# Kernel tuning notes

Hardware: AMD Instinct MI355X
Metric: run time of the kernel (lower is better)

The kernel has to match this reference:

```python
import jax, jax.numpy as jnp
import numpy as np
import math

D_MODEL = 640
HEAD_DIM = 64
N_HEADS = 14
N_KV_HEADS = 2
HPK = N_HEADS // N_KV_HEADS  # 7
EPS = 1e-5
T = 2048
D_HALF = HEAD_DIM // 2


def setup_inputs() -> dict:
    key = jax.random.key(0)
    ks = jax.random.split(key, 10)
    x = jax.random.normal(ks[0], (1, D_MODEL, 1, T), dtype=jnp.float32)
    # rope tables: realistic cos/sin from standard rotary frequencies
    inv_freq = 1.0 / (10000.0 ** (jnp.arange(0, HEAD_DIM, 2, dtype=jnp.float32) / HEAD_DIM))
    ang = jnp.arange(T, dtype=jnp.float32)[:, None] * inv_freq[None, :]  # (T, 32)
    rope_cos = jnp.cos(ang)
    rope_sin = jnp.sin(ang)
    # causal additive mask (T, T)
    causal = jnp.tril(jnp.ones((T, T), dtype=bool))
    attn_mask = jnp.where(causal, 0.0, -1e9).astype(jnp.float32)
    norm_w = 1.0 + 0.02 * jax.random.normal(ks[1], (D_MODEL,), dtype=jnp.float32)
    qkv_dim = (N_HEADS + 2 * N_KV_HEADS) * HEAD_DIM  # 1152
    qkv_w = jax.random.normal(ks[2], (qkv_dim, D_MODEL), dtype=jnp.float32) * (D_MODEL ** -0.5)
    qkv_b = 0.02 * jax.random.normal(ks[3], (qkv_dim,), dtype=jnp.float32)
    o_w = jax.random.normal(ks[4], (D_MODEL, N_HEADS * HEAD_DIM), dtype=jnp.float32) * ((N_HEADS * HEAD_DIM) ** -0.5)
    o_b = 0.02 * jax.random.normal(ks[5], (D_MODEL,), dtype=jnp.float32)
    sinks = jax.random.normal(ks[6], (N_HEADS,), dtype=jnp.float32)
    return {"x": x, "rope_cos": rope_cos, "rope_sin": rope_sin, "attn_mask": attn_mask,
            "norm_w": norm_w, "qkv_w": qkv_w, "qkv_b": qkv_b, "o_w": o_w, "o_b": o_b,
            "sinks": sinks}


def _apply_rope(xf, n_heads, rope_cos, rope_sin):
    # xf: (1, T, n_heads*dh) -> interleaved rotary
    xr = xf.reshape(1, T, n_heads, HEAD_DIM)
    x1 = xr[..., 0::2]  # (1, T, n, d_half)
    x2 = xr[..., 1::2]
    cos = rope_cos[None, :, None, :]
    sin = rope_sin[None, :, None, :]
    o1 = x1 * cos - x2 * sin
    o2 = x2 * cos + x1 * sin
    return jnp.stack((o1, o2), axis=-1).reshape(1, T, n_heads * HEAD_DIM)


def reference(x, rope_cos, rope_sin, attn_mask, norm_w, qkv_w, qkv_b, o_w, o_b, sinks):
    nh, nkv, hpk, dh = N_HEADS, N_KV_HEADS, HPK, HEAD_DIM
    residual = x
    # RMSNorm over channel dim (axis=1)
    var = jnp.mean(x * x, axis=1, keepdims=True)
    normed = x * jax.lax.rsqrt(var + EPS) * norm_w.reshape(1, -1, 1, 1)
    # fused 1x1 conv QKV: (1, D, T) -> (1, T, qkv_dim)
    n2 = normed[:, :, 0, :]  # (1, D, T)
    qkv = jnp.einsum('bct,oc->bto', n2, qkv_w) + qkv_b
    q_dim = nh * dh
    kv_dim = nkv * dh
    q = qkv[:, :, :q_dim]
    k = qkv[:, :, q_dim:q_dim + kv_dim]
    v = qkv[:, :, q_dim + kv_dim:]
    q = _apply_rope(q, nh, rope_cos, rope_sin)
    k = _apply_rope(k, nkv, rope_cos, rope_sin)
    qk_scale = 1.0 / math.sqrt(math.sqrt(dh))
    q = q * qk_scale
    k = k * qk_scale
    q = q.reshape(1, T, nkv, hpk, dh)
    k = k.reshape(1, T, nkv, dh)
    v = v.reshape(1, T, nkv, dh)
    # GQA scores: (1, nkv, hpk, T, T)
    scores = jnp.einsum('btkgd,bskd->bkgts', q, k)
    scores = scores + attn_mask[None, None, None, :, :]
    # attention-sink logit column appended before softmax
    sink = (sinks * math.log(2.0)).reshape(1, nkv, hpk, 1, 1)
    sink_col = jnp.broadcast_to(sink, (1, nkv, hpk, T, 1))
    scores_with_sink = jnp.concatenate([scores, sink_col], axis=-1)
    attn_w = jax.nn.softmax(scores_with_sink, axis=-1)[..., :-1]
    # weighted values: (1, T, nkv, hpk, dh) -> (1, T, nh*dh)
    attn_out = jnp.einsum('bkgts,bskd->btkgd', attn_w, v).reshape(1, T, nh * dh)
    # output 1x1 conv + residual
    proj = jnp.einsum('bto,do->bdt', attn_out, o_w) + o_b.reshape(1, -1, 1)
    return residual + proj[:, :, None, :]
```

## Files before the change

kernel.cpp:

```cpp
#include <hip/hip_runtime.h>
#include <math.h>

#define T 2048
#define DM 640
#define NH 14
#define NKV 2
#define HPK 7
#define HD 64
#define QDIM 896
#define QKV_DIM 1152

constexpr float QK_SCALE = 0.35355339059327373f;
constexpr float LN2F = 0.6931471805599453f;
constexpr float EPSF = 1e-5f;

typedef __attribute__((ext_vector_type(8))) short short8;
typedef __attribute__((ext_vector_type(4))) float float4v;

static __device__ __forceinline__ unsigned short f2bf(float f) {
    union { float f; unsigned u; } v; v.f = f;
    unsigned r = v.u + 0x7fffu + ((v.u >> 16) & 1u);
    return (unsigned short)(r >> 16);
}
static __device__ __forceinline__ float bf2f(unsigned short s) {
    union { unsigned u; float f; } v; v.u = ((unsigned)s) << 16;
    return v.f;
}

__global__ __launch_bounds__(256) void rstd_partial_kernel(
    const float* __restrict__ x, float* __restrict__ rpart)
{
    const int t = blockIdx.x * 256 + threadIdx.x;
    const int cb = blockIdx.y;
    float ss = 0.f;
    #pragma unroll 8
    for (int i = 0; i < 64; ++i) {
        float v = x[(cb * 64 + i) * T + t];
        ss = fmaf(v, v, ss);
    }
    rpart[cb * T + t] = ss;
}

__global__ __launch_bounds__(256) void rstd_final_kernel(
    const float* __restrict__ rpart, float* __restrict__ rstd)
{
    const int t = blockIdx.x * 256 + threadIdx.x;
    float ss = 0.f;
    #pragma unroll
    for (int j = 0; j < 10; ++j) ss += rpart[j * T + t];
    rstd[t] = rsqrtf(ss * (1.0f / DM) + EPSF);
}

__global__ __launch_bounds__(256) void cast_hilo_kernel(
    const float* __restrict__ in, unsigned short* __restrict__ hi,
    unsigned short* __restrict__ lo, int n4)
{
    for (int i = blockIdx.x * 256 + threadIdx.x; i < n4; i += gridDim.x * 256) {
        const float4 v = ((const float4*)in)[i];
        ushort4 h, l;
        h.x = f2bf(v.x); l.x = f2bf(v.x - bf2f(h.x));
        h.y = f2bf(v.y); l.y = f2bf(v.y - bf2f(h.y));
        h.z = f2bf(v.z); l.z = f2bf(v.z - bf2f(h.z));
        h.w = f2bf(v.w); l.w = f2bf(v.w - bf2f(h.w));
        ((ushort4*)hi)[i] = h;
        ((ushort4*)lo)[i] = l;
    }
}

__global__ __launch_bounds__(256) void xnorm_kernel(
    const float* __restrict__ x, const float* __restrict__ norm_w,
    const float* __restrict__ rstd,
    unsigned short* __restrict__ XnH, unsigned short* __restrict__ XnL)
{
    const int tid = threadIdx.x;
    const int t0 = blockIdx.x * 64;
    const int c0 = blockIdx.y * 64;
    __shared__ float xs[64][65];

    #pragma unroll
    for (int it = 0; it < 4; ++it) {
        const int r = (tid >> 4) + it * 16;
        const int cl = (tid & 15) * 4;
        const float4 v = *(const float4*)&x[(size_t)(c0 + r) * T + t0 + cl];
        xs[r][cl + 0] = v.x; xs[r][cl + 1] = v.y;
        xs[r][cl + 2] = v.z; xs[r][cl + 3] = v.w;
    }
    __syncthreads();
    #pragma unroll
    for (int it = 0; it < 4; ++it) {
        const int tr = (tid >> 4) + it * 16;
        const int cl = (tid & 15) * 4;
        const float rs = rstd[t0 + tr];
        ushort4 h, l;
        float v0 = xs[cl + 0][tr] * norm_w[c0 + cl + 0] * rs;
        float v1 = xs[cl + 1][tr] * norm_w[c0 + cl + 1] * rs;
        float v2 = xs[cl + 2][tr] * norm_w[c0 + cl + 2] * rs;
        float v3 = xs[cl + 3][tr] * norm_w[c0 + cl + 3] * rs;
        h.x = f2bf(v0); l.x = f2bf(v0 - bf2f(h.x));
        h.y = f2bf(v1); l.y = f2bf(v1 - bf2f(h.y));
        h.z = f2bf(v2); l.z = f2bf(v2 - bf2f(h.z));
        h.w = f2bf(v3); l.w = f2bf(v3 - bf2f(h.w));
        *(ushort4*)&XnH[(size_t)(t0 + tr) * DM + c0 + cl] = h;
        *(ushort4*)&XnL[(size_t)(t0 + tr) * DM + c0 + cl] = l;
    }
}

#define QSX_H 0
#define QSX_L 8192
#define QSW_H 16384
#define QSW_L 24576

__global__ __launch_bounds__(256) void qkv_mfma_kernel(
    const unsigned short* __restrict__ XnH, const unsigned short* __restrict__ XnL,
    const unsigned short* __restrict__ WH, const unsigned short* __restrict__ WL,
    const float* __restrict__ qkv_b, const float* __restrict__ rope_cos,
    const float* __restrict__ rope_sin,
    unsigned short* __restrict__ Qh, unsigned short* __restrict__ Ql,
    unsigned short* __restrict__ Kh, unsigned short* __restrict__ Kl,
    unsigned short* __restrict__ Vth, unsigned short* __restrict__ Vtl)
{
    const int t0 = blockIdx.x * 64;
    const int o0 = blockIdx.y * 64;
    const int tid = threadIdx.x;
    const int wave = tid >> 6, lane = tid & 63;
    const int lg = lane >> 4, lq = lane & 15;
    const int wr = wave >> 1, wc = wave & 1;

    __shared__ __align__(16) unsigned char sm[32768];

    float4v acc[2][2];
    acc[0][0] = (float4v)0.f; acc[0][1] = (float4v)0.f;
    acc[1][0] = (float4v)0.f; acc[1][1] = (float4v)0.f;

    for (int c0 = 0; c0 < DM; c0 += 64) {
        __syncthreads();
        #pragma unroll
        for (int rep = 0; rep < 2; ++rep) {
            const int ci = tid + rep * 256;
            const int row = ci >> 3, cc = ci & 7;
            const int dst = row * 128 + ((cc * 16) ^ ((row & 7) << 4));
            *(uint4*)(sm + QSX_H + dst) = *(const uint4*)&XnH[(size_t)(t0 + row) * DM + c0 + cc * 8];
            *(uint4*)(sm + QSX_L + dst) = *(const uint4*)&XnL[(size_t)(t0 + row) * DM + c0 + cc * 8];
            *(uint4*)(sm + QSW_H + dst) = *(const uint4*)&WH[(size_t)(o0 + row) * DM + c0 + cc * 8];
            *(uint4*)(sm + QSW_L + dst) = *(const uint4*)&WL[(size_t)(o0 + row) * DM + c0 + cc * 8];
        }
        __syncthreads();
        #pragma unroll
        for (int kk = 0; kk < 2; ++kk) {
            short8 ah[2], al[2], bh[2], bl[2];
            #pragma unroll
            for (int nt = 0; nt < 2; ++nt) {
                const int row = wc * 32 + nt * 16 + lq;
                const int col = (kk * 64 + lg * 16) ^ ((row & 7) << 4);
                bh[nt] = *(const short8*)(sm + QSX_H + row * 128 + col);
                bl[nt] = *(const short8*)(sm + QSX_L + row * 128 + col);
            }
            #pragma unroll
            for (int mt = 0; mt < 2; ++mt) {
                const int row = wr * 32 + mt * 16 + lq;
                const int col = (kk * 64 + lg * 16) ^ ((row & 7) << 4);
                ah[mt] = *(const short8*)(sm + QSW_H + row * 128 + col);
                al[mt] = *(const short8*)(sm + QSW_L + row * 128 + col);
            }
            #pragma unroll
            for (int mt = 0; mt < 2; ++mt) {
                #pragma unroll
                for (int nt = 0; nt < 2; ++nt) {
                    acc[mt][nt] = __builtin_amdgcn_mfma_f32_16x16x32_bf16(ah[mt], bh[nt], acc[mt][nt], 0, 0, 0);
                    acc[mt][nt] = __builtin_amdgcn_mfma_f32_16x16x32_bf16(ah[mt], bl[nt], acc[mt][nt], 0, 0, 0);
                    acc[mt][nt] = __builtin_amdgcn_mfma_f32_16x16x32_bf16(al[mt], bh[nt], acc[mt][nt], 0, 0, 0);
                }
            }
        }
    }

    const int by = blockIdx.y;
    #pragma unroll
    for (int mt = 0; mt < 2; ++mt) {
        const int d0 = wr * 32 + mt * 16 + lg * 4;
        #pragma unroll
        for (int nt = 0; nt < 2; ++nt) {
            const int t = t0 + wc * 32 + nt * 16 + lq;
            if (by < 16) {
                const float e0 = acc[mt][nt][0] + qkv_b[o0 + d0 + 0];
                const float d1 = acc[mt][nt][1] + qkv_b[o0 + d0 + 1];
                const float e2 = acc[mt][nt][2] + qkv_b[o0 + d0 + 2];
                const float d3 = acc[mt][nt][3] + qkv_b[o0 + d0 + 3];
                const float c0v = rope_cos[t * 32 + (d0 >> 1)];
                const float s0v = rope_sin[t * 32 + (d0 >> 1)];
                const float c1v = rope_cos[t * 32 + (d0 >> 1) + 1];
                const float s1v = rope_sin[t * 32 + (d0 >> 1) + 1];
                const float r0 = (e0 * c0v - d1 * s0v) * QK_SCALE;
                const float r1 = (d1 * c0v + e0 * s0v) * QK_SCALE;
                const float r2 = (e2 * c1v - d3 * s1v) * QK_SCALE;
                const float r3 = (d3 * c1v + e2 * s1v) * QK_SCALE;
                ushort4 h, l;
                h.x = f2bf(r0); l.x = f2bf(r0 - bf2f(h.x));
                h.y = f2bf(r1); l.y = f2bf(r1 - bf2f(h.y));
                h.z = f2bf(r2); l.z = f2bf(r2 - bf2f(h.z));
                h.w = f2bf(r3); l.w = f2bf(r3 - bf2f(h.w));
                if (by < 14) {
                    *(ushort4*)&Qh[((size_t)(by * T + t)) * HD + d0] = h;
                    *(ushort4*)&Ql[((size_t)(by * T + t)) * HD + d0] = l;
                } else {
                    const int h2 = by - 14;
                    *(ushort4*)&Kh[((size_t)(h2 * T + t)) * HD + d0] = h;
                    *(ushort4*)&Kl[((size_t)(h2 * T + t)) * HD + d0] = l;
                }
            } else {
                const int h2 = by - 16;
                #pragma unroll
                for (int j = 0; j < 4; ++j) {
                    const float val = acc[mt][nt][j] + qkv_b[o0 + d0 + j];
                    const unsigned short hh = f2bf(val);
                    Vth[((size_t)(h2 * HD + d0 + j)) * T + t] = hh;
                    Vtl[((size_t)(h2 * HD + d0 + j)) * T + t] = f2bf(val - bf2f(hh));
                }
            }
        }
    }
}

#define SK_H 0
#define SK_L 8192
#define SV_H 16384
#define SV_L 24576

__global__ __launch_bounds__(256) void attn_mfma_kernel(
    const unsigned short* __restrict__ Qh, const unsigned short* __restrict__ Ql,
    const unsigned short* __restrict__ Kh, const unsigned short* __restrict__ Kl,
    const unsigned short* __restrict__ Vth, const unsigned short* __restrict__ Vtl,
    const float* __restrict__ sinks,
    float* __restrict__ Opart, float* __restrict__ Mpart, float* __restrict__ Lpart)
{
    const int qt = blockIdx.x;
    const int h  = blockIdx.y;
    const int kc = blockIdx.z;
    if (qt < kc * 8) return;

    const int kvh = h / HPK;
    const int tid = threadIdx.x;
    const int wave = tid >> 6, lane = tid & 63;
    const int lg = lane >> 4, lq = lane & 15;
    const int qbase = qt * 64 + wave * 16;
    const int myq = qbase + lq;

    __shared__ __align__(16) unsigned char sm[32768];

    short8 qf[2][2];
    #pragma unroll
    for (int kk = 0; kk < 2; ++kk) {
        const size_t qoff = ((size_t)(h * T + myq)) * HD + kk * 32 + lg * 8;
        qf[kk][0] = *(const short8*)&Qh[qoff];
        qf[kk][1] = *(const short8*)&Ql[qoff];
    }

    float4v oacc[4];
    #pragma unroll
    for (int dt = 0; dt < 4; ++dt) oacc[dt] = (float4v)0.f;

    float m, l;
    if (kc == 0) { m = sinks[h] * LN2F; l = 1.0f; }
    else         { m = -3e38f;          l = 0.0f; }

    const unsigned short* Khp = Kh + ((size_t)kvh) * T * HD;
    const unsigned short* Klp = Kl + ((size_t)kvh) * T * HD;
    const unsigned short* Vhp = Vth + ((size_t)kvh) * HD * T;
    const unsigned short* Vlp = Vtl + ((size_t)kvh) * HD * T;

    const int kstart = kc * 512;
    const int kend = min(kstart + 512, qt * 64 + 64);

    for (int kb = kstart; kb < kend; kb += 64) {
        __syncthreads();
        #pragma unroll
        for (int rep = 0; rep < 2; ++rep) {
            const int ci = tid + rep * 256;
            const int row = ci >> 3, cc = ci & 7;
            const int dst = row * 128 + ((cc * 16) ^ ((row & 7) << 4));
            *(uint4*)(sm + SK_H + dst) = *(const uint4*)(Khp + (size_t)(kb + row) * HD + cc * 8);
            *(uint4*)(sm + SK_L + dst) = *(const uint4*)(Klp + (size_t)(kb + row) * HD + cc * 8);
            *(uint4*)(sm + SV_H + dst) = *(const uint4*)(Vhp + (size_t)row * T + kb + cc * 8);
            *(uint4*)(sm + SV_L + dst) = *(const uint4*)(Vlp + (size_t)row * T + kb + cc * 8);
        }
        __syncthreads();

        float4v st[4];
        #pragma unroll
        for (int t = 0; t < 4; ++t) st[t] = (float4v)0.f;
        #pragma unroll
        for (int t = 0; t < 4; ++t) {
            const int row = t * 16 + lq;
            const int sw = (row & 7) << 4;
            #pragma unroll
            for (int kk = 0; kk < 2; ++kk) {
                const int col = (kk * 64 + lg * 16) ^ sw;
                short8 ah = *(const short8*)(sm + SK_H + row * 128 + col);
                short8 al = *(const short8*)(sm + SK_L + row * 128 + col);
                st[t] = __builtin_amdgcn_mfma_f32_16x16x32_bf16(ah, qf[kk][0], st[t], 0, 0, 0);
                st[t] = __builtin_amdgcn_mfma_f32_16x16x32_bf16(ah, qf[kk][1], st[t], 0, 0, 0);
                st[t] = __builtin_amdgcn_mfma_f32_16x16x32_bf16(al, qf[kk][0], st[t], 0, 0, 0);
            }
        }

        float pmax = -3e38f;
        #pragma unroll
        for (int t = 0; t < 4; ++t) {
            #pragma unroll
            for (int j = 0; j < 4; ++j) {
                const int key = kb + 16 * t + 4 * lg + j;
                float s = st[t][j] + ((key > myq) ? -1e9f : 0.f);
                st[t][j] = s;
                pmax = fmaxf(pmax, s);
            }
        }
        pmax = fmaxf(pmax, __shfl_xor(pmax, 16));
        pmax = fmaxf(pmax, __shfl_xor(pmax, 32));
        const float mnew = fmaxf(m, pmax);
        const float corr = __expf(m - mnew);
        float psum = 0.f;
        #pragma unroll
        for (int t = 0; t < 4; ++t) {
            #pragma unroll
            for (int j = 0; j < 4; ++j) {
                const float p = __expf(st[t][j] - mnew);
                st[t][j] = p;
                psum += p;
            }
        }
        psum += __shfl_xor(psum, 16);
        psum += __shfl_xor(psum, 32);
        l = l * corr + psum;
        m = mnew;
        #pragma unroll
        for (int dt = 0; dt < 4; ++dt) oacc[dt] *= corr;

        #pragma unroll
        for (int c = 0; c < 2; ++c) {
            float pv[8];
            #pragma unroll
            for (int i = 0; i < 8; ++i) {
                const int j = i & 3;
                const int gsel = ((lg * 8 + i) >> 2) & 3;
                const int src = (gsel << 4) | lq;
                const float v0 = __shfl(st[2 * c + 0][j], src);
                const float v1 = __shfl(st[2 * c + 1][j], src);
                pv[i] = (lg >= 2) ? v1 : v0;
            }
            short8 ph, pl;
            #pragma unroll
            for (int i = 0; i < 8; ++i) {
                const unsigned short hi = f2bf(pv[i]);
                ph[i] = (short)hi;
                pl[i] = (short)f2bf(pv[i] - bf2f(hi));
            }
            #pragma unroll
            for (int dt = 0; dt < 4; ++dt) {
                const int row = dt * 16 + lq;
                const int col = (c * 64 + lg * 16) ^ ((row & 7) << 4);
                short8 vh = *(const short8*)(sm + SV_H + row * 128 + col);
                short8 vl = *(const short8*)(sm + SV_L + row * 128 + col);
                oacc[dt] = __builtin_amdgcn_mfma_f32_16x16x32_bf16(vh, ph, oacc[dt], 0, 0, 0);
                oacc[dt] = __builtin_amdgcn_mfma_f32_16x16x32_bf16(vh, pl, oacc[dt], 0, 0, 0);
                oacc[dt] = __builtin_amdgcn_mfma_f32_16x16x32_bf16(vl, ph, oacc[dt], 0, 0, 0);
            }
        }
    }

    const int r = qbase + lq;
    const int pb = (h * 4 + kc) * 64;
    #pragma unroll
    for (int dt = 0; dt < 4; ++dt) {
        #pragma unroll
        for (int j = 0; j < 4; ++j) {
            const int d = dt * 16 + lg * 4 + j;
            Opart[(size_t)(pb + d) * T + r] = oacc[dt][j];
        }
    }
    if (lane < 16) {
        Mpart[(size_t)(h * 4 + kc) * T + r] = m;
        Lpart[(size_t)(h * 4 + kc) * T + r] = l;
    }
}

__global__ __launch_bounds__(256) void attn_combine_kernel(
    const float* __restrict__ Opart, const float* __restrict__ Mpart,
    const float* __restrict__ Lpart,
    unsigned short* __restrict__ AOH, unsigned short* __restrict__ AOL)
{
    const int idx = blockIdx.x * 256 + threadIdx.x;
    const int h = idx >> 11;
    const int r = idx & (T - 1);
    const int nch = (r >> 9) + 1;

    float mv0, mv1 = -3e38f, mv2 = -3e38f, mv3 = -3e38f;
    float lv0, lv1 = 0.f, lv2 = 0.f, lv3 = 0.f;
    mv0 = Mpart[(h * 4 + 0) * T + r]; lv0 = Lpart[(h * 4 + 0) * T + r];
    if (nch > 1) { mv1 = Mpart[(h * 4 + 1) * T + r]; lv1 = Lpart[(h * 4 + 1) * T + r]; }
    if (nch > 2) { mv2 = Mpart[(h * 4 + 2) * T + r]; lv2 = Lpart[(h * 4 + 2) * T + r]; }
    if (nch > 3) { mv3 = Mpart[(h * 4 + 3) * T + r]; lv3 = Lpart[(h * 4 + 3) * T + r]; }
    const float M = fmaxf(fmaxf(mv0, mv1), fmaxf(mv2, mv3));
    float w0 = __expf(mv0 - M), w1 = __expf(mv1 - M);
    float w2 = __expf(mv2 - M), w3 = __expf(mv3 - M);
    const float L = lv0 * w0 + lv1 * w1 + lv2 * w2 + lv3 * w3;
    const float invL = 1.0f / L;
    w0 *= invL; w1 *= invL; w2 *= invL; w3 *= invL;

    #pragma unroll
    for (int d4 = 0; d4 < 16; ++d4) {
        ushort4 hh, ll;
        #pragma unroll
        for (int j = 0; j < 4; ++j) {
            const int d = d4 * 4 + j;
            float acc = Opart[((h * 4 + 0) * 64 + d) * (size_t)T + r] * w0;
            if (nch > 1) acc = fmaf(Opart[((h * 4 + 1) * 64 + d) * (size_t)T + r], w1, acc);
            if (nch > 2) acc = fmaf(Opart[((h * 4 + 2) * 64 + d) * (size_t)T + r], w2, acc);
            if (nch > 3) acc = fmaf(Opart[((h * 4 + 3) * 64 + d) * (size_t)T + r], w3, acc);
            const unsigned short hv = f2bf(acc);
            ((unsigned short*)&hh)[j] = hv;
            ((unsigned short*)&ll)[j] = f2bf(acc - bf2f(hv));
        }
        *(ushort4*)&AOH[(size_t)r * QDIM + h * 64 + d4 * 4] = hh;
        *(ushort4*)&AOL[(size_t)r * QDIM + h * 64 + d4 * 4] = ll;
    }
}

#define PSA_H 0
#define PSA_L 8192
#define PSW_H 16384
#define PSW_L 24576

__global__ __launch_bounds__(256) void oproj_mfma_kernel(
    const unsigned short* __restrict__ AOH, const unsigned short* __restrict__ AOL,
    const unsigned short* __restrict__ OWH, const unsigned short* __restrict__ OWL,
    const float* __restrict__ o_b, const float* __restrict__ x,
    float* __restrict__ out)
{
    const int t0 = blockIdx.x * 64;
    const int c0 = blockIdx.y * 64;
    const int tid = threadIdx.x;
    const int wave = tid >> 6, lane = tid & 63;
    const int lg = lane >> 4, lq = lane & 15;
    const int wr = wave >> 1, wc = wave & 1;

    __shared__ __align__(16) unsigned char sm[32768];

    float4v acc[2][2];
    acc[0][0] = (float4v)0.f; acc[0][1] = (float4v)0.f;
    acc[1][0] = (float4v)0.f; acc[1][1] = (float4v)0.f;

    for (int k0 = 0; k0 < QDIM; k0 += 64) {
        __syncthreads();
        #pragma unroll
        for (int rep = 0; rep < 2; ++rep) {
            const int ci = tid + rep * 256;
            const int row = ci >> 3, cc = ci & 7;
            const int dst = row * 128 + ((cc * 16) ^ ((row & 7) << 4));
            *(uint4*)(sm + PSA_H + dst) = *(const uint4*)&AOH[(size_t)(t0 + row) * QDIM + k0 + cc * 8];
            *(uint4*)(sm + PSA_L + dst) = *(const uint4*)&AOL[(size_t)(t0 + row) * QDIM + k0 + cc * 8];
            *(uint4*)(sm + PSW_H + dst) = *(const uint4*)&OWH[(size_t)(c0 + row) * QDIM + k0 + cc * 8];
            *(uint4*)(sm + PSW_L + dst) = *(const uint4*)&OWL[(size_t)(c0 + row) * QDIM + k0 + cc * 8];
        }
        __syncthreads();
        #pragma unroll
        for (int kk = 0; kk < 2; ++kk) {
            short8 ah[2], al[2], bh[2], bl[2];
            #pragma unroll
            for (int nt = 0; nt < 2; ++nt) {
                const int row = wc * 32 + nt * 16 + lq;
                const int col = (kk * 64 + lg * 16) ^ ((row & 7) << 4);
                bh[nt] = *(const short8*)(sm + PSA_H + row * 128 + col);
                bl[nt] = *(const short8*)(sm + PSA_L + row * 128 + col);
            }
            #pragma unroll
            for (int mt = 0; mt < 2; ++mt) {
                const int row = wr * 32 + mt * 16 + lq;
                const int col = (kk * 64 + lg * 16) ^ ((row & 7) << 4);
                ah[mt] = *(const short8*)(sm + PSW_H + row * 128 + col);
                al[mt] = *(const short8*)(sm + PSW_L + row * 128 + col);
            }
            #pragma unroll
            for (int mt = 0; mt < 2; ++mt) {
                #pragma unroll
                for (int nt = 0; nt < 2; ++nt) {
                    acc[mt][nt] = __builtin_amdgcn_mfma_f32_16x16x32_bf16(ah[mt], bh[nt], acc[mt][nt], 0, 0, 0);
                    acc[mt][nt] = __builtin_amdgcn_mfma_f32_16x16x32_bf16(ah[mt], bl[nt], acc[mt][nt], 0, 0, 0);
                    acc[mt][nt] = __builtin_amdgcn_mfma_f32_16x16x32_bf16(al[mt], bh[nt], acc[mt][nt], 0, 0, 0);
                }
            }
        }
    }

    #pragma unroll
    for (int mt = 0; mt < 2; ++mt) {
        const int cb = c0 + wr * 32 + mt * 16 + lg * 4;
        #pragma unroll
        for (int nt = 0; nt < 2; ++nt) {
            const int t = t0 + wc * 32 + nt * 16 + lq;
            #pragma unroll
            for (int j = 0; j < 4; ++j) {
                const int c = cb + j;
                out[(size_t)c * T + t] = acc[mt][nt][j] + o_b[c] + x[(size_t)c * T + t];
            }
        }
    }
}

extern "C" void kernel_launch(void* const* d_in, const int* in_sizes, int n_in,
                              void* d_out, int out_size, void* d_ws, size_t ws_size,
                              hipStream_t stream) {
    const float* x        = (const float*)d_in[0];
    const float* rope_cos = (const float*)d_in[1];
    const float* rope_sin = (const float*)d_in[2];
    const float* norm_w   = (const float*)d_in[4];
    const float* qkv_w    = (const float*)d_in[5];
    const float* qkv_b    = (const float*)d_in[6];
    const float* o_w      = (const float*)d_in[7];
    const float* o_b      = (const float*)d_in[8];
    const float* sinks    = (const float*)d_in[9];
    float* out = (float*)d_out;

    float* ws    = (float*)d_ws;
    float* rpart = ws;
    float* rstd  = rpart + 20480;
    float* Opart = rstd + 2048;
    float* Mpart = Opart + 7340032;
    float* Lpart = Mpart + 114688;
    unsigned short* bws = (unsigned short*)(Lpart + 114688);
    unsigned short* Qh  = bws;
    unsigned short* Ql  = Qh  + 1835008;
    unsigned short* Kh  = Ql  + 1835008;
    unsigned short* Kl  = Kh  + 262144;
    unsigned short* Vth = Kl  + 262144;
    unsigned short* Vtl = Vth + 262144;
    unsigned short* XnH = Vtl + 262144;
    unsigned short* XnL = XnH + 1310720;
    unsigned short* WqH = XnL + 1310720;
    unsigned short* WqL = WqH + 737280;
    unsigned short* OWH = WqL + 737280;
    unsigned short* OWL = OWH + 573440;
    unsigned short* AOH = OWL + 573440;
    unsigned short* AOL = AOH + 1835008;

    rstd_partial_kernel<<<dim3(8, 10), 256, 0, stream>>>(x, rpart);
    rstd_final_kernel<<<8, 256, 0, stream>>>(rpart, rstd);
    cast_hilo_kernel<<<720, 256, 0, stream>>>(qkv_w, WqH, WqL, QKV_DIM * DM / 4);
    cast_hilo_kernel<<<560, 256, 0, stream>>>(o_w, OWH, OWL, DM * QDIM / 4);
    xnorm_kernel<<<dim3(32, 10), 256, 0, stream>>>(x, norm_w, rstd, XnH, XnL);
    qkv_mfma_kernel<<<dim3(32, 18), 256, 0, stream>>>(
        XnH, XnL, WqH, WqL, qkv_b, rope_cos, rope_sin, Qh, Ql, Kh, Kl, Vth, Vtl);
    attn_mfma_kernel<<<dim3(32, NH, 4), 256, 0, stream>>>(
        Qh, Ql, Kh, Kl, Vth, Vtl, sinks, Opart, Mpart, Lpart);
    attn_combine_kernel<<<NH * T / 256, 256, 0, stream>>>(Opart, Mpart, Lpart, AOH, AOL);
    oproj_mfma_kernel<<<dim3(32, 10), 256, 0, stream>>>(AOH, AOL, OWH, OWL, o_b, x, out);
}
```

Measured before the change: 267.7 us.

## Double-buffer GEMM/attention tiles, drop split-K attention combine, merge small prep kernels

Adds register-staged double buffering of LDS tiles in the QKV, attention and output-projection kernels, so global loads for the next tile overlap MFMA work on the current one. Attention no longer splits along keys into partial outputs plus a combine kernel. Each block handles all keys for its query tile, walks query tiles in reverse to schedule long rows first, uses an exp2-based softmax with log2e folded into the Q scale, and writes bf16 hi/lo output directly. The rstd reduction is merged into one kernel and the two weight casts into one launch. Trade-offs are doubled LDS use, which lowers occupancy, and less parallelism in attention for short causal rows.

```diff
diff --git a/kernel.cpp b/kernel.cpp
--- a/kernel.cpp
+++ b/kernel.cpp
@@ -10,67 +10,64 @@
 #define QDIM 896
 #define QKV_DIM 1152
 
-constexpr float QK_SCALE = 0.35355339059327373f;
-constexpr float LN2F = 0.6931471805599453f;
+constexpr float QK_SCALE2 = 0.35355339059327373f * 1.2011224087864498f;
 constexpr float EPSF = 1e-5f;
 
 typedef __attribute__((ext_vector_type(8))) short short8;
 typedef __attribute__((ext_vector_type(4))) float float4v;
-
-static __device__ __forceinline__ unsigned short f2bf(float f) {
+typedef unsigned short ush;
+
+static __device__ __forceinline__ ush f2bf(float f) {
     union { float f; unsigned u; } v; v.f = f;
     unsigned r = v.u + 0x7fffu + ((v.u >> 16) & 1u);
-    return (unsigned short)(r >> 16);
-}
-static __device__ __forceinline__ float bf2f(unsigned short s) {
+    return (ush)(r >> 16);
+}
+static __device__ __forceinline__ float bf2f(ush s) {
     union { unsigned u; float f; } v; v.u = ((unsigned)s) << 16;
     return v.f;
 }
 
-__global__ __launch_bounds__(256) void rstd_partial_kernel(
-    const float* __restrict__ x, float* __restrict__ rpart)
+__global__ __launch_bounds__(256) void rstd_kernel(
+    const float* __restrict__ x, float* __restrict__ rstd)
 {
-    const int t = blockIdx.x * 256 + threadIdx.x;
-    const int cb = blockIdx.y;
+    const int t0 = blockIdx.x * 64;
+    const int tl = threadIdx.x & 63, cg = threadIdx.x >> 6;
+    __shared__ float red[4][64];
     float ss = 0.f;
-    #pragma unroll 8
-    for (int i = 0; i < 64; ++i) {
-        float v = x[(cb * 64 + i) * T + t];
+    for (int c = cg; c < DM; c += 4) {
+        const float v = x[(size_t)c * T + t0 + tl];
         ss = fmaf(v, v, ss);
     }
-    rpart[cb * T + t] = ss;
-}
-
-__global__ __launch_bounds__(256) void rstd_final_kernel(
-    const float* __restrict__ rpart, float* __restrict__ rstd)
+    red[cg][tl] = ss;
+    __syncthreads();
+    if (threadIdx.x < 64) {
+        const float s = red[0][tl] + red[1][tl] + red[2][tl] + red[3][tl];
+        rstd[t0 + tl] = rsqrtf(s * (1.0f / DM) + EPSF);
+    }
+}
+
+__global__ __launch_bounds__(256) void cast2_kernel(
+    const float* __restrict__ a, ush* __restrict__ ah, ush* __restrict__ al, int na4,
+    const float* __restrict__ b, ush* __restrict__ bh, ush* __restrict__ bl)
 {
-    const int t = blockIdx.x * 256 + threadIdx.x;
-    float ss = 0.f;
-    #pragma unroll
-    for (int j = 0; j < 10; ++j) ss += rpart[j * T + t];
-    rstd[t] = rsqrtf(ss * (1.0f / DM) + EPSF);
-}
-
-__global__ __launch_bounds__(256) void cast_hilo_kernel(
-    const float* __restrict__ in, unsigned short* __restrict__ hi,
-    unsigned short* __restrict__ lo, int n4)
-{
-    for (int i = blockIdx.x * 256 + threadIdx.x; i < n4; i += gridDim.x * 256) {
-        const float4 v = ((const float4*)in)[i];
-        ushort4 h, l;
-        h.x = f2bf(v.x); l.x = f2bf(v.x - bf2f(h.x));
-        h.y = f2bf(v.y); l.y = f2bf(v.y - bf2f(h.y));
-        h.z = f2bf(v.z); l.z = f2bf(v.z - bf2f(h.z));
-        h.w = f2bf(v.w); l.w = f2bf(v.w - bf2f(h.w));
-        ((ushort4*)hi)[i] = h;
-        ((ushort4*)lo)[i] = l;
-    }
+    const int i = blockIdx.x * 256 + threadIdx.x;
+    const float* src; ush *dh, *dl; int j;
+    if (i < na4) { src = a; dh = ah; dl = al; j = i; }
+    else         { src = b; dh = bh; dl = bl; j = i - na4; }
+    const float4 v = ((const float4*)src)[j];
+    ushort4 h, l;
+    h.x = f2bf(v.x); l.x = f2bf(v.x - bf2f(h.x));
+    h.y = f2bf(v.y); l.y = f2bf(v.y - bf2f(h.y));
+    h.z = f2bf(v.z); l.z = f2bf(v.z - bf2f(h.z));
+    h.w = f2bf(v.w); l.w = f2bf(v.w - bf2f(h.w));
+    ((ushort4*)dh)[j] = h;
+    ((ushort4*)dl)[j] = l;
 }
 
 __global__ __launch_bounds__(256) void xnorm_kernel(
     const float* __restrict__ x, const float* __restrict__ norm_w,
     const float* __restrict__ rstd,
-    unsigned short* __restrict__ XnH, unsigned short* __restrict__ XnL)
+    ush* __restrict__ XnH, ush* __restrict__ XnL)
 {
     const int tid = threadIdx.x;
     const int t0 = blockIdx.x * 64;
@@ -92,10 +89,10 @@
         const int cl = (tid & 15) * 4;
         const float rs = rstd[t0 + tr];
         ushort4 h, l;
-        float v0 = xs[cl + 0][tr] * norm_w[c0 + cl + 0] * rs;
-        float v1 = xs[cl + 1][tr] * norm_w[c0 + cl + 1] * rs;
-        float v2 = xs[cl + 2][tr] * norm_w[c0 + cl + 2] * rs;
-        float v3 = xs[cl + 3][tr] * norm_w[c0 + cl + 3] * rs;
+        const float v0 = xs[cl + 0][tr] * norm_w[c0 + cl + 0] * rs;
+        const float v1 = xs[cl + 1][tr] * norm_w[c0 + cl + 1] * rs;
+        const float v2 = xs[cl + 2][tr] * norm_w[c0 + cl + 2] * rs;
+        const float v3 = xs[cl + 3][tr] * norm_w[c0 + cl + 3] * rs;
         h.x = f2bf(v0); l.x = f2bf(v0 - bf2f(h.x));
         h.y = f2bf(v1); l.y = f2bf(v1 - bf2f(h.y));
         h.z = f2bf(v2); l.z = f2bf(v2 - bf2f(h.z));
@@ -111,13 +108,13 @@
 #define QSW_L 24576
 
 __global__ __launch_bounds__(256) void qkv_mfma_kernel(
-    const unsigned short* __restrict__ XnH, const unsigned short* __restrict__ XnL,
-    const unsigned short* __restrict__ WH, const unsigned short* __restrict__ WL,
+    const ush* __restrict__ XnH, const ush* __restrict__ XnL,
+    const ush* __restrict__ WH, const ush* __restrict__ WL,
     const float* __restrict__ qkv_b, const float* __restrict__ rope_cos,
     const float* __restrict__ rope_sin,
-    unsigned short* __restrict__ Qh, unsigned short* __restrict__ Ql,
-    unsigned short* __restrict__ Kh, unsigned short* __restrict__ Kl,
-    unsigned short* __restrict__ Vth, unsigned short* __restrict__ Vtl)
+    ush* __restrict__ Qh, ush* __restrict__ Ql,
+    ush* __restrict__ Kh, ush* __restrict__ Kl,
+    ush* __restrict__ Vth, ush* __restrict__ Vtl)
 {
     const int t0 = blockIdx.x * 64;
     const int o0 = blockIdx.y * 64;
@@ -126,25 +123,47 @@
     const int lg = lane >> 4, lq = lane & 15;
     const int wr = wave >> 1, wc = wave & 1;
 
-    __shared__ __align__(16) unsigned char sm[32768];
+    __shared__ __align__(16) unsigned char sm[65536];
+
+    const int srow0 = tid >> 3, srow1 = srow0 + 32, scc = tid & 7;
+    const int dst0 = srow0 * 128 + ((scc * 16) ^ ((srow0 & 7) << 4));
+    const int dst1 = srow1 * 128 + ((scc * 16) ^ ((srow1 & 7) << 4));
+
+    uint4 xh0, xl0, wh0, wl0, xh1, xl1, wh1, wl1;
+
+#define QLOAD(c_) do { \
+    xh0 = *(const uint4*)&XnH[(size_t)(t0 + srow0) * DM + (c_) + scc * 8]; \
+    xl0 = *(const uint4*)&XnL[(size_t)(t0 + srow0) * DM + (c_) + scc * 8]; \
+    wh0 = *(const uint4*)&WH [(size_t)(o0 + srow0) * DM + (c_) + scc * 8]; \
+    wl0 = *(const uint4*)&WL [(size_t)(o0 + srow0) * DM + (c_) + scc * 8]; \
+    xh1 = *(const uint4*)&XnH[(size_t)(t0 + srow1) * DM + (c_) + scc * 8]; \
+    xl1 = *(const uint4*)&XnL[(size_t)(t0 + srow1) * DM + (c_) + scc * 8]; \
+    wh1 = *(const uint4*)&WH [(size_t)(o0 + srow1) * DM + (c_) + scc * 8]; \
+    wl1 = *(const uint4*)&WL [(size_t)(o0 + srow1) * DM + (c_) + scc * 8]; \
+} while (0)
+
+#define QSTORE(b_) do { \
+    *(uint4*)((b_) + QSX_H + dst0) = xh0; \
+    *(uint4*)((b_) + QSX_L + dst0) = xl0; \
+    *(uint4*)((b_) + QSW_H + dst0) = wh0; \
+    *(uint4*)((b_) + QSW_L + dst0) = wl0; \
+    *(uint4*)((b_) + QSX_H + dst1) = xh1; \
+    *(uint4*)((b_) + QSX_L + dst1) = xl1; \
+    *(uint4*)((b_) + QSW_H + dst1) = wh1; \
+    *(uint4*)((b_) + QSW_L + dst1) = wl1; \
+} while (0)
 
     float4v acc[2][2];
     acc[0][0] = (float4v)0.f; acc[0][1] = (float4v)0.f;
     acc[1][0] = (float4v)0.f; acc[1][1] = (float4v)0.f;
 
-    for (int c0 = 0; c0 < DM; c0 += 64) {
+    QLOAD(0);
+    QSTORE(sm);
+    int cur = 0;
+    for (int s = 0; s < 10; ++s) {
+        if (s < 9) QLOAD((s + 1) * 64);
         __syncthreads();
-        #pragma unroll
-        for (int rep = 0; rep < 2; ++rep) {
-            const int ci = tid + rep * 256;
-            const int row = ci >> 3, cc = ci & 7;
-            const int dst = row * 128 + ((cc * 16) ^ ((row & 7) << 4));
-            *(uint4*)(sm + QSX_H + dst) = *(const uint4*)&XnH[(size_t)(t0 + row) * DM + c0 + cc * 8];
-            *(uint4*)(sm + QSX_L + dst) = *(const uint4*)&XnL[(size_t)(t0 + row) * DM + c0 + cc * 8];
-            *(uint4*)(sm + QSW_H + dst) = *(const uint4*)&WH[(size_t)(o0 + row) * DM + c0 + cc * 8];
-            *(uint4*)(sm + QSW_L + dst) = *(const uint4*)&WL[(size_t)(o0 + row) * DM + c0 + cc * 8];
-        }
-        __syncthreads();
+        const unsigned char* smb = sm + cur * 32768;
         #pragma unroll
         for (int kk = 0; kk < 2; ++kk) {
             short8 ah[2], al[2], bh[2], bl[2];
@@ -152,15 +171,15 @@
             for (int nt = 0; nt < 2; ++nt) {
                 const int row = wc * 32 + nt * 16 + lq;
                 const int col = (kk * 64 + lg * 16) ^ ((row & 7) << 4);
-                bh[nt] = *(const short8*)(sm + QSX_H + row * 128 + col);
-                bl[nt] = *(const short8*)(sm + QSX_L + row * 128 + col);
+                bh[nt] = *(const short8*)(smb + QSX_H + row * 128 + col);
+                bl[nt] = *(const short8*)(smb + QSX_L + row * 128 + col);
             }
             #pragma unroll
             for (int mt = 0; mt < 2; ++mt) {
                 const int row = wr * 32 + mt * 16 + lq;
                 const int col = (kk * 64 + lg * 16) ^ ((row & 7) << 4);
-                ah[mt] = *(const short8*)(sm + QSW_H + row * 128 + col);
-                al[mt] = *(const short8*)(sm + QSW_L + row * 128 + col);
+                ah[mt] = *(const short8*)(smb + QSW_H + row * 128 + col);
+                al[mt] = *(const short8*)(smb + QSW_L + row * 128 + col);
             }
             #pragma unroll
             for (int mt = 0; mt < 2; ++mt) {
@@ -172,7 +191,10 @@
                 }
             }
         }
-    }
+        if (s < 9) { QSTORE(sm + ((cur ^ 1) * 32768)); cur ^= 1; }
+    }
+#undef QLOAD
+#undef QSTORE
 
     const int by = blockIdx.y;
     #pragma unroll
@@ -190,10 +212,10 @@
                 const float s0v = rope_sin[t * 32 + (d0 >> 1)];
                 const float c1v = rope_cos[t * 32 + (d0 >> 1) + 1];
                 const float s1v = rope_sin[t * 32 + (d0 >> 1) + 1];
-                const float r0 = (e0 * c0v - d1 * s0v) * QK_SCALE;
-                const float r1 = (d1 * c0v + e0 * s0v) * QK_SCALE;
-                const float r2 = (e2 * c1v - d3 * s1v) * QK_SCALE;
-                const float r3 = (d3 * c1v + e2 * s1v) * QK_SCALE;
+                const float r0 = (e0 * c0v - d1 * s0v) * QK_SCALE2;
+                const float r1 = (d1 * c0v + e0 * s0v) * QK_SCALE2;
+                const float r2 = (e2 * c1v - d3 * s1v) * QK_SCALE2;
+                const float r3 = (d3 * c1v + e2 * s1v) * QK_SCALE2;
                 ushort4 h, l;
                 h.x = f2bf(r0); l.x = f2bf(r0 - bf2f(h.x));
                 h.y = f2bf(r1); l.y = f2bf(r1 - bf2f(h.y));
@@ -212,7 +234,7 @@
                 #pragma unroll
                 for (int j = 0; j < 4; ++j) {
                     const float val = acc[mt][nt][j] + qkv_b[o0 + d0 + j];
-                    const unsigned short hh = f2bf(val);
+                    const ush hh = f2bf(val);
                     Vth[((size_t)(h2 * HD + d0 + j)) * T + t] = hh;
                     Vtl[((size_t)(h2 * HD + d0 + j)) * T + t] = f2bf(val - bf2f(hh));
                 }
@@ -221,23 +243,15 @@
     }
 }
 
-#define SK_H 0
-#define SK_L 8192
-#define SV_H 16384
-#define SV_L 24576
-
 __global__ __launch_bounds__(256) void attn_mfma_kernel(
-    const unsigned short* __restrict__ Qh, const unsigned short* __restrict__ Ql,
-    const unsigned short* __restrict__ Kh, const unsigned short* __restrict__ Kl,
-    const unsigned short* __restrict__ Vth, const unsigned short* __restrict__ Vtl,
+    const ush* __restrict__ Qh, const ush* __restrict__ Ql,
+    const ush* __restrict__ Kh, const ush* __restrict__ Kl,
+    const ush* __restrict__ Vth, const ush* __restrict__ Vtl,
     const float* __restrict__ sinks,
-    float* __restrict__ Opart, float* __restrict__ Mpart, float* __restrict__ Lpart)
+    ush* __restrict__ AOH, ush* __restrict__ AOL)
 {
-    const int qt = blockIdx.x;
+    const int qt = 31 - (int)blockIdx.x;
     const int h  = blockIdx.y;
-    const int kc = blockIdx.z;
-    if (qt < kc * 8) return;
-
     const int kvh = h / HPK;
     const int tid = threadIdx.x;
     const int wave = tid >> 6, lane = tid & 63;
@@ -245,7 +259,8 @@
     const int qbase = qt * 64 + wave * 16;
     const int myq = qbase + lq;
 
-    __shared__ __align__(16) unsigned char sm[32768];
+    __shared__ __align__(16) unsigned char sm[2 * 32768 + 4 * 2304];
+    unsigned int* Pl = (unsigned int*)(sm + 65536) + wave * (16 * 36);
 
     short8 qf[2][2];
     #pragma unroll
@@ -259,31 +274,52 @@
     #pragma unroll
     for (int dt = 0; dt < 4; ++dt) oacc[dt] = (float4v)0.f;
 
-    float m, l;
-    if (kc == 0) { m = sinks[h] * LN2F; l = 1.0f; }
-    else         { m = -3e38f;          l = 0.0f; }
-
-    const unsigned short* Khp = Kh + ((size_t)kvh) * T * HD;
-    const unsigned short* Klp = Kl + ((size_t)kvh) * T * HD;
-    const unsigned short* Vhp = Vth + ((size_t)kvh) * HD * T;
-    const unsigned short* Vlp = Vtl + ((size_t)kvh) * HD * T;
-
-    const int kstart = kc * 512;
-    const int kend = min(kstart + 512, qt * 64 + 64);
-
-    for (int kb = kstart; kb < kend; kb += 64) {
+    float m2 = sinks[h];
+    float l  = 1.0f;
+
+    const ush* Khp = Kh + (size_t)kvh * T * HD;
+    const ush* Klp = Kl + (size_t)kvh * T * HD;
+    const ush* Vhp = Vth + (size_t)kvh * HD * T;
+    const ush* Vlp = Vtl + (size_t)kvh * HD * T;
+
+    const int srow0 = tid >> 3, srow1 = srow0 + 32, scc = tid & 7;
+    const int dst0 = srow0 * 128 + ((scc * 16) ^ ((srow0 & 7) << 4));
+    const int dst1 = srow1 * 128 + ((scc * 16) ^ ((srow1 & 7) << 4));
+
+    uint4 rk0h, rk0l, rv0h, rv0l, rk1h, rk1l, rv1h, rv1l;
+
+#define ALOAD(kb_) do { \
+    rk0h = *(const uint4*)(Khp + (size_t)((kb_) + srow0) * HD + scc * 8); \
+    rk0l = *(const uint4*)(Klp + (size_t)((kb_) + srow0) * HD + scc * 8); \
+    rv0h = *(const uint4*)(Vhp + (size_t)srow0 * T + (kb_) + scc * 8); \
+    rv0l = *(const uint4*)(Vlp + (size_t)srow0 * T + (kb_) + scc * 8); \
+    rk1h = *(const uint4*)(Khp + (size_t)((kb_) + srow1) * HD + scc * 8); \
+    rk1l = *(const uint4*)(Klp + (size_t)((kb_) + srow1) * HD + scc * 8); \
+    rv1h = *(const uint4*)(Vhp + (size_t)srow1 * T + (kb_) + scc * 8); \
+    rv1l = *(const uint4*)(Vlp + (size_t)srow1 * T + (kb_) + scc * 8); \
+} while (0)
+
+#define ASTORE(b_) do { \
+    *(uint4*)((b_) + 0     + dst0) = rk0h; \
+    *(uint4*)((b_) + 8192  + dst0) = rk0l; \
+    *(uint4*)((b_) + 16384 + dst0) = rv0h; \
+    *(uint4*)((b_) + 24576 + dst0) = rv0l; \
+    *(uint4*)((b_) + 0     + dst1) = rk1h; \
+    *(uint4*)((b_) + 8192  + dst1) = rk1l; \
+    *(uint4*)((b_) + 16384 + dst1) = rv1h; \
+    *(uint4*)((b_) + 24576 + dst1) = rv1l; \
+} while (0)
+
+    ALOAD(0);
+    ASTORE(sm);
+    int cur = 0;
+
+    for (int kt = 0; kt <= qt; ++kt) {
+        const int kb = kt * 64;
+        const bool more = (kt < qt);
+        if (more) ALOAD(kb + 64);
         __syncthreads();
-        #pragma unroll
-        for (int rep = 0; rep < 2; ++rep) {
-            const int ci = tid + rep * 256;
-            const int row = ci >> 3, cc = ci & 7;
-            const int dst = row * 128 + ((cc * 16) ^ ((row & 7) << 4));
-            *(uint4*)(sm + SK_H + dst) = *(const uint4*)(Khp + (size_t)(kb + row) * HD + cc * 8);
-            *(uint4*)(sm + SK_L + dst) = *(const uint4*)(Klp + (size_t)(kb + row) * HD + cc * 8);
-            *(uint4*)(sm + SV_H + dst) = *(const uint4*)(Vhp + (size_t)row * T + kb + cc * 8);
-            *(uint4*)(sm + SV_L + dst) = *(const uint4*)(Vlp + (size_t)row * T + kb + cc * 8);
-        }
-        __syncthreads();
+        unsigned char* smb = sm + cur * 32768;
 
         float4v st[4];
         #pragma unroll
@@ -291,12 +327,13 @@
         #pragma unroll
         for (int t = 0; t < 4; ++t) {
             const int row = t * 16 + lq;
+            const int rb = row * 128;
             const int sw = (row & 7) << 4;
             #pragma unroll
             for (int kk = 0; kk < 2; ++kk) {
                 const int col = (kk * 64 + lg * 16) ^ sw;
-                short8 ah = *(const short8*)(sm + SK_H + row * 128 + col);
-                short8 al = *(const short8*)(sm + SK_L + row * 128 + col);
+                const short8 ah = *(const short8*)(smb + rb + col);
+                const short8 al = *(const short8*)(smb + 8192 + rb + col);
                 st[t] = __builtin_amdgcn_mfma_f32_16x16x32_bf16(ah, qf[kk][0], st[t], 0, 0, 0);
                 st[t] = __builtin_amdgcn_mfma_f32_16x16x32_bf16(ah, qf[kk][1], st[t], 0, 0, 0);
                 st[t] = __builtin_amdgcn_mfma_f32_16x16x32_bf16(al, qf[kk][0], st[t], 0, 0, 0);
@@ -309,119 +346,80 @@
             #pragma unroll
             for (int j = 0; j < 4; ++j) {
                 const int key = kb + 16 * t + 4 * lg + j;
-                float s = st[t][j] + ((key > myq) ? -1e9f : 0.f);
+                const float s = (key > myq) ? -3e38f : st[t][j];
                 st[t][j] = s;
                 pmax = fmaxf(pmax, s);
             }
         }
         pmax = fmaxf(pmax, __shfl_xor(pmax, 16));
         pmax = fmaxf(pmax, __shfl_xor(pmax, 32));
-        const float mnew = fmaxf(m, pmax);
-        const float corr = __expf(m - mnew);
+        if (__any(pmax > m2)) {
+            const float mnew = fmaxf(m2, pmax);
+            const float corr = exp2f(m2 - mnew);
+            l *= corr;
+            #pragma unroll
+            for (int dt = 0; dt < 4; ++dt) oacc[dt] *= corr;
+            m2 = mnew;
+        }
         float psum = 0.f;
         #pragma unroll
         for (int t = 0; t < 4; ++t) {
             #pragma unroll
             for (int j = 0; j < 4; ++j) {
-                const float p = __expf(st[t][j] - mnew);
+                const float p = exp2f(st[t][j] - m2);
                 st[t][j] = p;
                 psum += p;
             }
         }
         psum += __shfl_xor(psum, 16);
         psum += __shfl_xor(psum, 32);
-        l = l * corr + psum;
-        m = mnew;
-        #pragma unroll
-        for (int dt = 0; dt < 4; ++dt) oacc[dt] *= corr;
+        l += psum;
+
+        #pragma unroll
+        for (int t = 0; t < 4; ++t) {
+            #pragma unroll
+            for (int j2 = 0; j2 < 2; ++j2) {
+                const unsigned int u = (unsigned int)f2bf(st[t][2 * j2]) |
+                                       ((unsigned int)f2bf(st[t][2 * j2 + 1]) << 16);
+                Pl[lq * 36 + t * 8 + lg * 2 + j2] = u;
+            }
+        }
 
         #pragma unroll
         for (int c = 0; c < 2; ++c) {
-            float pv[8];
-            #pragma unroll
-            for (int i = 0; i < 8; ++i) {
-                const int j = i & 3;
-                const int gsel = ((lg * 8 + i) >> 2) & 3;
-                const int src = (gsel << 4) | lq;
-                const float v0 = __shfl(st[2 * c + 0][j], src);
-                const float v1 = __shfl(st[2 * c + 1][j], src);
-                pv[i] = (lg >= 2) ? v1 : v0;
-            }
-            short8 ph, pl;
-            #pragma unroll
-            for (int i = 0; i < 8; ++i) {
-                const unsigned short hi = f2bf(pv[i]);
-                ph[i] = (short)hi;
-                pl[i] = (short)f2bf(pv[i] - bf2f(hi));
-            }
+            const short8 pf = *(const short8*)&Pl[lq * 36 + c * 16 + lg * 4];
             #pragma unroll
             for (int dt = 0; dt < 4; ++dt) {
                 const int row = dt * 16 + lq;
+                const int rb = row * 128;
                 const int col = (c * 64 + lg * 16) ^ ((row & 7) << 4);
-                short8 vh = *(const short8*)(sm + SV_H + row * 128 + col);
-                short8 vl = *(const short8*)(sm + SV_L + row * 128 + col);
-                oacc[dt] = __builtin_amdgcn_mfma_f32_16x16x32_bf16(vh, ph, oacc[dt], 0, 0, 0);
-                oacc[dt] = __builtin_amdgcn_mfma_f32_16x16x32_bf16(vh, pl, oacc[dt], 0, 0, 0);
-                oacc[dt] = __builtin_amdgcn_mfma_f32_16x16x32_bf16(vl, ph, oacc[dt], 0, 0, 0);
-            }
-        }
-    }
-
+                const short8 vh = *(const short8*)(smb + 16384 + rb + col);
+                const short8 vl = *(const short8*)(smb + 24576 + rb + col);
+                oacc[dt] = __builtin_amdgcn_mfma_f32_16x16x32_bf16(vh, pf, oacc[dt], 0, 0, 0);
+                oacc[dt] = __builtin_amdgcn_mfma_f32_16x16x32_bf16(vl, pf, oacc[dt], 0, 0, 0);
+            }
+        }
+
+        if (more) { ASTORE(sm + ((cur ^ 1) * 32768)); cur ^= 1; }
+    }
+#undef ALOAD
+#undef ASTORE
+
+    const float invl = 1.0f / l;
     const int r = qbase + lq;
-    const int pb = (h * 4 + kc) * 64;
+    const size_t obase = (size_t)r * QDIM + h * 64;
     #pragma unroll
     for (int dt = 0; dt < 4; ++dt) {
+        ushort4 hh, ll;
         #pragma unroll
         for (int j = 0; j < 4; ++j) {
-            const int d = dt * 16 + lg * 4 + j;
-            Opart[(size_t)(pb + d) * T + r] = oacc[dt][j];
-        }
-    }
-    if (lane < 16) {
-        Mpart[(size_t)(h * 4 + kc) * T + r] = m;
-        Lpart[(size_t)(h * 4 + kc) * T + r] = l;
-    }
-}
-
-__global__ __launch_bounds__(256) void attn_combine_kernel(
-    const float* __restrict__ Opart, const float* __restrict__ Mpart,
-    const float* __restrict__ Lpart,
-    unsigned short* __restrict__ AOH, unsigned short* __restrict__ AOL)
-{
-    const int idx = blockIdx.x * 256 + threadIdx.x;
-    const int h = idx >> 11;
-    const int r = idx & (T - 1);
-    const int nch = (r >> 9) + 1;
-
-    float mv0, mv1 = -3e38f, mv2 = -3e38f, mv3 = -3e38f;
-    float lv0, lv1 = 0.f, lv2 = 0.f, lv3 = 0.f;
-    mv0 = Mpart[(h * 4 + 0) * T + r]; lv0 = Lpart[(h * 4 + 0) * T + r];
-    if (nch > 1) { mv1 = Mpart[(h * 4 + 1) * T + r]; lv1 = Lpart[(h * 4 + 1) * T + r]; }
-    if (nch > 2) { mv2 = Mpart[(h * 4 + 2) * T + r]; lv2 = Lpart[(h * 4 + 2) * T + r]; }
-    if (nch > 3) { mv3 = Mpart[(h * 4 + 3) * T + r]; lv3 = Lpart[(h * 4 + 3) * T + r]; }
-    const float M = fmaxf(fmaxf(mv0, mv1), fmaxf(mv2, mv3));
-    float w0 = __expf(mv0 - M), w1 = __expf(mv1 - M);
-    float w2 = __expf(mv2 - M), w3 = __expf(mv3 - M);
-    const float L = lv0 * w0 + lv1 * w1 + lv2 * w2 + lv3 * w3;
-    const float invL = 1.0f / L;
-    w0 *= invL; w1 *= invL; w2 *= invL; w3 *= invL;
-
-    #pragma unroll
-    for (int d4 = 0; d4 < 16; ++d4) {
-        ushort4 hh, ll;
-        #pragma unroll
-        for (int j = 0; j < 4; ++j) {
-            const int d = d4 * 4 + j;
-            float acc = Opart[((h * 4 + 0) * 64 + d) * (size_t)T + r] * w0;
-            if (nch > 1) acc = fmaf(Opart[((h * 4 + 1) * 64 + d) * (size_t)T + r], w1, acc);
-            if (nch > 2) acc = fmaf(Opart[((h * 4 + 2) * 64 + d) * (size_t)T + r], w2, acc);
-            if (nch > 3) acc = fmaf(Opart[((h * 4 + 3) * 64 + d) * (size_t)T + r], w3, acc);
-            const unsigned short hv = f2bf(acc);
-            ((unsigned short*)&hh)[j] = hv;
-            ((unsigned short*)&ll)[j] = f2bf(acc - bf2f(hv));
-        }
-        *(ushort4*)&AOH[(size_t)r * QDIM + h * 64 + d4 * 4] = hh;
-        *(ushort4*)&AOL[(size_t)r * QDIM + h * 64 + d4 * 4] = ll;
+            const float val = oacc[dt][j] * invl;
+            const ush hv = f2bf(val);
+            ((ush*)&hh)[j] = hv;
+            ((ush*)&ll)[j] = f2bf(val - bf2f(hv));
+        }
+        *(ushort4*)&AOH[obase + dt * 16 + lg * 4] = hh;
+        *(ushort4*)&AOL[obase + dt * 16 + lg * 4] = ll;
     }
 }
 
@@ -431,8 +429,8 @@
 #define PSW_L 24576
 
 __global__ __launch_bounds__(256) void oproj_mfma_kernel(
-    const unsigned short* __restrict__ AOH, const unsigned short* __restrict__ AOL,
-    const unsigned short* __restrict__ OWH, const unsigned short* __restrict__ OWL,
+    const ush* __restrict__ AOH, const ush* __restrict__ AOL,
+    const ush* __restrict__ OWH, const ush* __restrict__ OWL,
     const float* __restrict__ o_b, const float* __restrict__ x,
     float* __restrict__ out)
 {
@@ -443,25 +441,47 @@
     const int lg = lane >> 4, lq = lane & 15;
     const int wr = wave >> 1, wc = wave & 1;
 
-    __shared__ __align__(16) unsigned char sm[32768];
+    __shared__ __align__(16) unsigned char sm[65536];
+
+    const int srow0 = tid >> 3, srow1 = srow0 + 32, scc = tid & 7;
+    const int dst0 = srow0 * 128 + ((scc * 16) ^ ((srow0 & 7) << 4));
+    const int dst1 = srow1 * 128 + ((scc * 16) ^ ((srow1 & 7) << 4));
+
+    uint4 xh0, xl0, wh0, wl0, xh1, xl1, wh1, wl1;
+
+#define PLOAD(k_) do { \
+    xh0 = *(const uint4*)&AOH[(size_t)(t0 + srow0) * QDIM + (k_) + scc * 8]; \
+    xl0 = *(const uint4*)&AOL[(size_t)(t0 + srow0) * QDIM + (k_) + scc * 8]; \
+    wh0 = *(const uint4*)&OWH[(size_t)(c0 + srow0) * QDIM + (k_) + scc * 8]; \
+    wl0 = *(const uint4*)&OWL[(size_t)(c0 + srow0) * QDIM + (k_) + scc * 8]; \
+    xh1 = *(const uint4*)&AOH[(size_t)(t0 + srow1) * QDIM + (k_) + scc * 8]; \
+    xl1 = *(const uint4*)&AOL[(size_t)(t0 + srow1) * QDIM + (k_) + scc * 8]; \
+    wh1 = *(const uint4*)&OWH[(size_t)(c0 + srow1) * QDIM + (k_) + scc * 8]; \
+    wl1 = *(const uint4*)&OWL[(size_t)(c0 + srow1) * QDIM + (k_) + scc * 8]; \
+} while (0)
+
+#define PSTORE(b_) do { \
+    *(uint4*)((b_) + PSA_H + dst0) = xh0; \
+    *(uint4*)((b_) + PSA_L + dst0) = xl0; \
+    *(uint4*)((b_) + PSW_H + dst0) = wh0; \
+    *(uint4*)((b_) + PSW_L + dst0) = wl0; \
+    *(uint4*)((b_) + PSA_H + dst1) = xh1; \
+    *(uint4*)((b_) + PSA_L + dst1) = xl1; \
+    *(uint4*)((b_) + PSW_H + dst1) = wh1; \
+    *(uint4*)((b_) + PSW_L + dst1) = wl1; \
+} while (0)
 
     float4v acc[2][2];
     acc[0][0] = (float4v)0.f; acc[0][1] = (float4v)0.f;
     acc[1][0] = (float4v)0.f; acc[1][1] = (float4v)0.f;
 
-    for (int k0 = 0; k0 < QDIM; k0 += 64) {
+    PLOAD(0);
+    PSTORE(sm);
+    int cur = 0;
+    for (int s = 0; s < 14; ++s) {
+        if (s < 13) PLOAD((s + 1) * 64);
         __syncthreads();
-        #pragma unroll
-        for (int rep = 0; rep < 2; ++rep) {
-            const int ci = tid + rep * 256;
-            const int row = ci >> 3, cc = ci & 7;
-            const int dst = row * 128 + ((cc * 16) ^ ((row & 7) << 4));
-            *(uint4*)(sm + PSA_H + dst) = *(const uint4*)&AOH[(size_t)(t0 + row) * QDIM + k0 + cc * 8];
-            *(uint4*)(sm + PSA_L + dst) = *(const uint4*)&AOL[(size_t)(t0 + row) * QDIM + k0 + cc * 8];
-            *(uint4*)(sm + PSW_H + dst) = *(const uint4*)&OWH[(size_t)(c0 + row) * QDIM + k0 + cc * 8];
-            *(uint4*)(sm + PSW_L + dst) = *(const uint4*)&OWL[(size_t)(c0 + row) * QDIM + k0 + cc * 8];
-        }
-        __syncthreads();
+        const unsigned char* smb = sm + cur * 32768;
         #pragma unroll
         for (int kk = 0; kk < 2; ++kk) {
             short8 ah[2], al[2], bh[2], bl[2];
@@ -469,15 +489,15 @@
             for (int nt = 0; nt < 2; ++nt) {
                 const int row = wc * 32 + nt * 16 + lq;
                 const int col = (kk * 64 + lg * 16) ^ ((row & 7) << 4);
-                bh[nt] = *(const short8*)(sm + PSA_H + row * 128 + col);
-                bl[nt] = *(const short8*)(sm + PSA_L + row * 128 + col);
+                bh[nt] = *(const short8*)(smb + PSA_H + row * 128 + col);
+                bl[nt] = *(const short8*)(smb + PSA_L + row * 128 + col);
             }
             #pragma unroll
             for (int mt = 0; mt < 2; ++mt) {
                 const int row = wr * 32 + mt * 16 + lq;
                 const int col = (kk * 64 + lg * 16) ^ ((row & 7) << 4);
-                ah[mt] = *(const short8*)(sm + PSW_H + row * 128 + col);
-                al[mt] = *(const short8*)(sm + PSW_L + row * 128 + col);
+                ah[mt] = *(const short8*)(smb + PSW_H + row * 128 + col);
+                al[mt] = *(const short8*)(smb + PSW_L + row * 128 + col);
             }
             #pragma unroll
             for (int mt = 0; mt < 2; ++mt) {
@@ -489,7 +509,10 @@
                 }
             }
         }
-    }
+        if (s < 13) { PSTORE(sm + ((cur ^ 1) * 32768)); cur ^= 1; }
+    }
+#undef PLOAD
+#undef PSTORE
 
     #pragma unroll
     for (int mt = 0; mt < 2; ++mt) {
@@ -520,37 +543,31 @@
     const float* sinks    = (const float*)d_in[9];
     float* out = (float*)d_out;
 
-    float* ws    = (float*)d_ws;
-    float* rpart = ws;
-    float* rstd  = rpart + 20480;
-    float* Opart = rstd + 2048;
-    float* Mpart = Opart + 7340032;
-    float* Lpart = Mpart + 114688;
-    unsigned short* bws = (unsigned short*)(Lpart + 114688);
-    unsigned short* Qh  = bws;
-    unsigned short* Ql  = Qh  + 1835008;
-    unsigned short* Kh  = Ql  + 1835008;
-    unsigned short* Kl  = Kh  + 262144;
-    unsigned short* Vth = Kl  + 262144;
-    unsigned short* Vtl = Vth + 262144;
-    unsigned short* XnH = Vtl + 262144;
-    unsigned short* XnL = XnH + 1310720;
-    unsigned short* WqH = XnL + 1310720;
-    unsigned short* WqL = WqH + 737280;
-    unsigned short* OWH = WqL + 737280;
-    unsigned short* OWL = OWH + 573440;
-    unsigned short* AOH = OWL + 573440;
-    unsigned short* AOL = AOH + 1835008;
-
-    rstd_partial_kernel<<<dim3(8, 10), 256, 0, stream>>>(x, rpart);
-    rstd_final_kernel<<<8, 256, 0, stream>>>(rpart, rstd);
-    cast_hilo_kernel<<<720, 256, 0, stream>>>(qkv_w, WqH, WqL, QKV_DIM * DM / 4);
-    cast_hilo_kernel<<<560, 256, 0, stream>>>(o_w, OWH, OWL, DM * QDIM / 4);
+    float* ws   = (float*)d_ws;
+    float* rstd = ws;
+    ush* bws = (ush*)(rstd + 2048);
+    ush* Qh  = bws;
+    ush* Ql  = Qh  + 1835008;
+    ush* Kh  = Ql  + 1835008;
+    ush* Kl  = Kh  + 262144;
+    ush* Vth = Kl  + 262144;
+    ush* Vtl = Vth + 262144;
+    ush* XnH = Vtl + 262144;
+    ush* XnL = XnH + 1310720;
+    ush* WqH = XnL + 1310720;
+    ush* WqL = WqH + 737280;
+    ush* OWH = WqL + 737280;
+    ush* OWL = OWH + 573440;
+    ush* AOH = OWL + 573440;
+    ush* AOL = AOH + 1835008;
+
+    rstd_kernel<<<32, 256, 0, stream>>>(x, rstd);
+    cast2_kernel<<<1280, 256, 0, stream>>>(qkv_w, WqH, WqL, QKV_DIM * DM / 4,
+                                           o_w, OWH, OWL);
     xnorm_kernel<<<dim3(32, 10), 256, 0, stream>>>(x, norm_w, rstd, XnH, XnL);
     qkv_mfma_kernel<<<dim3(32, 18), 256, 0, stream>>>(
         XnH, XnL, WqH, WqL, qkv_b, rope_cos, rope_sin, Qh, Ql, Kh, Kl, Vth, Vtl);
-    attn_mfma_kernel<<<dim3(32, NH, 4), 256, 0, stream>>>(
-        Qh, Ql, Kh, Kl, Vth, Vtl, sinks, Opart, Mpart, Lpart);
-    attn_combine_kernel<<<NH * T / 256, 256, 0, stream>>>(Opart, Mpart, Lpart, AOH, AOL);
+    attn_mfma_kernel<<<dim3(32, NH), 256, 0, stream>>>(
+        Qh, Ql, Kh, Kl, Vth, Vtl, sinks, AOH, AOL);
     oproj_mfma_kernel<<<dim3(32, 10), 256, 0, stream>>>(AOH, AOL, OWH, OWL, o_b, x, out);
 }
```

Measured after the change: 250.8 us. 6.3% less time.
